# Performance work log

Hardware: AMD Instinct MI355X
Metric: run time of the kernel (lower is better)

The kernel has to match this reference:

```python
import jax, jax.numpy as jnp
import numpy as np

R = 16
ALPHA = 1
SCALING = ALPHA / R
IN_M, IN_N = 64, 64    # factorization(4096)
OUT_L, OUT_K = 64, 64  # factorization(4096)


def setup_inputs() -> dict:
    key = jax.random.key(0)
    k_x, k1a, k1b, k2a, k2b = jax.random.split(key, 5)
    x = jax.random.normal(k_x, (8192, 4096), dtype=jnp.float32)
    # lokr_w1_a: (r, out_l), lokr_w1_b: (in_m, r), lokr_w2_a: (r, out_k), lokr_w2_b: (in_n, r)
    # (init_weights zeros w1_a; we use random values so the test exercises real math)
    s = 0.05
    w1_a = jax.random.normal(k1a, (R, OUT_L), dtype=jnp.float32) * s
    w1_b = jax.random.normal(k1b, (IN_M, R), dtype=jnp.float32) * s
    w2_a = jax.random.normal(k2a, (R, OUT_K), dtype=jnp.float32) * s
    w2_b = jax.random.normal(k2b, (IN_N, R), dtype=jnp.float32) * s
    return {"x": x, "w1_a": w1_a, "w1_b": w1_b, "w2_a": w2_a, "w2_b": w2_b}


def reference(x, w1_a, w1_b, w2_a, w2_b):
    # w1 = w1_a^T @ w1_b^T -> (out_l, in_m); w2 = w2_a^T @ w2_b^T -> (out_k, in_n)
    w1 = w1_a.T @ w1_b.T
    w2 = w2_a.T @ w2_b.T
    # kron(w1^T, w2^T): (in_m*in_n, out_l*out_k) = (in_features, out_features)
    W = jnp.kron(w1.T, w2.T)
    # dropout rate is 0.0 -> identity
    return (x @ W) * SCALING
```

## Files before the change

### kernel.cpp

```cpp
#include <hip/hip_runtime.h>


typedef __fp16 h2 __attribute__((ext_vector_type(2)));
typedef __fp16 h4 __attribute__((ext_vector_type(4)));
typedef float  f4 __attribute__((ext_vector_type(4)));

__device__ __forceinline__ h4 pack4(float a, float b, float c, float d) {
    h2 lo = __builtin_amdgcn_cvt_pkrtz(a, b);
    h2 hi = __builtin_amdgcn_cvt_pkrtz(c, d);
    h4 r;
    r[0] = lo[0]; r[1] = lo[1]; r[2] = hi[0]; r[3] = hi[1];
    return r;
}

#define MFMA16(a, b, c) __builtin_amdgcn_mfma_f32_16x16x16f16((a), (b), (c), 0, 0, 0)

#define ROWS 2

__global__ __launch_bounds__(256) void lokr_kernel(
    const float* __restrict__ x,
    const float* __restrict__ w1_a,
    const float* __restrict__ w1_b,
    const float* __restrict__ w2_a,
    const float* __restrict__ w2_b,
    float* __restrict__ out)
{
    const int lane = threadIdx.x & 63;
    const int g    = lane >> 4;
    const int c    = lane & 15;
    const int gw   = blockIdx.x * 4 + (threadIdx.x >> 6);
    const size_t b0 = (size_t)gw * ROWS;

    h4 W1B[4], W2BT[4], W2A[4], W1AT[4];
#pragma unroll
    for (int t = 0; t < 4; ++t) {
        const int kb = t * 16 + g * 4;
        W1B[t]  = pack4(w1_b[(kb+0)*16 + c], w1_b[(kb+1)*16 + c],
                        w1_b[(kb+2)*16 + c], w1_b[(kb+3)*16 + c]);
        W2BT[t] = pack4(w2_b[(kb+0)*16 + c], w2_b[(kb+1)*16 + c],
                        w2_b[(kb+2)*16 + c], w2_b[(kb+3)*16 + c]);
        W2A[t]  = pack4(w2_a[(g*4+0)*64 + t*16 + c], w2_a[(g*4+1)*64 + t*16 + c],
                        w2_a[(g*4+2)*64 + t*16 + c], w2_a[(g*4+3)*64 + t*16 + c]);
        W1AT[t] = pack4(w1_a[(g*4+0)*64 + t*16 + c] * 0.0625f,
                        w1_a[(g*4+1)*64 + t*16 + c] * 0.0625f,
                        w1_a[(g*4+2)*64 + t*16 + c] * 0.0625f,
                        w1_a[(g*4+3)*64 + t*16 + c] * 0.0625f);
    }

    const f4 zero = {0.f, 0.f, 0.f, 0.f};

#pragma unroll 1
    for (int rr = 0; rr < ROWS; ++rr) {
        const float* xp = x + (b0 + rr) * 4096;

        float xf[4][4][4];
#pragma unroll
        for (int nt = 0; nt < 4; ++nt)
#pragma unroll
            for (int ks = 0; ks < 4; ++ks)
#pragma unroll
                for (int j = 0; j < 4; ++j)
                    xf[nt][ks][j] = xp[(ks*16 + g*4 + j)*64 + nt*16 + c];

        h4 XA[4][4];
#pragma unroll
        for (int nt = 0; nt < 4; ++nt)
#pragma unroll
            for (int ks = 0; ks < 4; ++ks)
                XA[nt][ks] = pack4(xf[nt][ks][0], xf[nt][ks][1],
                                   xf[nt][ks][2], xf[nt][ks][3]);

        f4 PT[4];
#pragma unroll
        for (int nt = 0; nt < 4; ++nt) {
            f4 acc = zero;
#pragma unroll
            for (int ks = 0; ks < 4; ++ks)
                acc = MFMA16(XA[nt][ks], W1B[ks], acc);
            PT[nt] = acc;
        }

        h4 PTH[4];
#pragma unroll
        for (int nt = 0; nt < 4; ++nt)
            PTH[nt] = pack4(PT[nt][0], PT[nt][1], PT[nt][2], PT[nt][3]);
        f4 qa = zero;
#pragma unroll
        for (int nt = 0; nt < 4; ++nt)
            qa = MFMA16(W2BT[nt], PTH[nt], qa);
        h4 QTH = pack4(qa[0], qa[1], qa[2], qa[3]);

        h4 UH[4];
#pragma unroll
        for (int kt = 0; kt < 4; ++kt) {
            f4 u = MFMA16(QTH, W2A[kt], zero);
            UH[kt] = pack4(u[0], u[1], u[2], u[3]);
        }

        float* op = out + (b0 + rr) * 4096 + g * 256 + c;
#pragma unroll
        for (int lt = 0; lt < 4; ++lt) {
#pragma unroll
            for (int kt = 0; kt < 4; ++kt) {
                f4 y = MFMA16(W1AT[lt], UH[kt], zero);
#pragma unroll
                for (int reg = 0; reg < 4; ++reg)
                    op[lt*1024 + reg*64 + kt*16] = y[reg];
            }
        }
    }
}

extern "C" void kernel_launch(void* const* d_in, const int* in_sizes, int n_in,
                              void* d_out, int out_size, void* d_ws, size_t ws_size,
                              hipStream_t stream) {
    const float* x    = (const float*)d_in[0];
    const float* w1_a = (const float*)d_in[1];
    const float* w1_b = (const float*)d_in[2];
    const float* w2_a = (const float*)d_in[3];
    const float* w2_b = (const float*)d_in[4];
    float* out = (float*)d_out;

    dim3 grid(1024), block(256);
    hipLaunchKernelGGL(lokr_kernel, grid, block, 0, stream,
                       x, w1_a, w1_b, w2_a, w2_b, out);
}
```

Baseline: 50.23 us.

## Reorder contraction to use vectorized x loads and prefetch second row

```diff
diff --git a/kernel.cpp b/kernel.cpp
--- a/kernel.cpp
+++ b/kernel.cpp
@@ -15,8 +15,6 @@
 
 #define MFMA16(a, b, c) __builtin_amdgcn_mfma_f32_16x16x16f16((a), (b), (c), 0, 0, 0)
 
-#define ROWS 2
-
 __global__ __launch_bounds__(256) void lokr_kernel(
     const float* __restrict__ x,
     const float* __restrict__ w1_a,
@@ -29,86 +27,88 @@
     const int g    = lane >> 4;
     const int c    = lane & 15;
     const int gw   = blockIdx.x * 4 + (threadIdx.x >> 6);
-    const size_t b0 = (size_t)gw * ROWS;
+    const size_t b0 = (size_t)gw * 2;
 
-    h4 W1B[4], W2BT[4], W2A[4], W1AT[4];
+    h4 W2B[4], W1BT[4], W1A[4], W2A[4];
 #pragma unroll
     for (int t = 0; t < 4; ++t) {
         const int kb = t * 16 + g * 4;
-        W1B[t]  = pack4(w1_b[(kb+0)*16 + c], w1_b[(kb+1)*16 + c],
+        W2B[t]  = pack4(w2_b[(kb+0)*16 + c], w2_b[(kb+1)*16 + c],
+                        w2_b[(kb+2)*16 + c], w2_b[(kb+3)*16 + c]);
+        W1BT[t] = pack4(w1_b[(kb+0)*16 + c], w1_b[(kb+1)*16 + c],
                         w1_b[(kb+2)*16 + c], w1_b[(kb+3)*16 + c]);
-        W2BT[t] = pack4(w2_b[(kb+0)*16 + c], w2_b[(kb+1)*16 + c],
-                        w2_b[(kb+2)*16 + c], w2_b[(kb+3)*16 + c]);
-        W2A[t]  = pack4(w2_a[(g*4+0)*64 + t*16 + c], w2_a[(g*4+1)*64 + t*16 + c],
-                        w2_a[(g*4+2)*64 + t*16 + c], w2_a[(g*4+3)*64 + t*16 + c]);
-        W1AT[t] = pack4(w1_a[(g*4+0)*64 + t*16 + c] * 0.0625f,
+        W1A[t]  = pack4(w1_a[(g*4+0)*64 + t*16 + c] * 0.0625f,
                         w1_a[(g*4+1)*64 + t*16 + c] * 0.0625f,
                         w1_a[(g*4+2)*64 + t*16 + c] * 0.0625f,
                         w1_a[(g*4+3)*64 + t*16 + c] * 0.0625f);
+        W2A[t]  = pack4(w2_a[(g*4+0)*64 + t*16 + c], w2_a[(g*4+1)*64 + t*16 + c],
+                        w2_a[(g*4+2)*64 + t*16 + c], w2_a[(g*4+3)*64 + t*16 + c]);
     }
 
     const f4 zero = {0.f, 0.f, 0.f, 0.f};
 
-#pragma unroll 1
-    for (int rr = 0; rr < ROWS; ++rr) {
-        const float* xp = x + (b0 + rr) * 4096;
+    const float* xp0 = x + b0 * 4096;
+    const float* xp1 = xp0 + 4096;
+    const int xoff = c * 64 + g * 4;
 
-        float xf[4][4][4];
+    auto compute_store = [&](const h4* XA, float* opb) {
+        f4 D1[4];
 #pragma unroll
-        for (int nt = 0; nt < 4; ++nt)
+        for (int mt = 0; mt < 4; ++mt) {
+            f4 a = zero;
 #pragma unroll
-            for (int ks = 0; ks < 4; ++ks)
+            for (int nk = 0; nk < 4; ++nk)
+                a = MFMA16(XA[mt * 4 + nk], W2B[nk], a);
+            D1[mt] = a;
+        }
+        f4 d2 = zero;
 #pragma unroll
-                for (int j = 0; j < 4; ++j)
-                    xf[nt][ks][j] = xp[(ks*16 + g*4 + j)*64 + nt*16 + c];
-
-        h4 XA[4][4];
+        for (int mt = 0; mt < 4; ++mt)
+            d2 = MFMA16(W1BT[mt], pack4(D1[mt][0], D1[mt][1], D1[mt][2], D1[mt][3]), d2);
+        h4 D2H = pack4(d2[0], d2[1], d2[2], d2[3]);
+        h4 D3H[4];
 #pragma unroll
-        for (int nt = 0; nt < 4; ++nt)
-#pragma unroll
-            for (int ks = 0; ks < 4; ++ks)
-                XA[nt][ks] = pack4(xf[nt][ks][0], xf[nt][ks][1],
-                                   xf[nt][ks][2], xf[nt][ks][3]);
-
-        f4 PT[4];
-#pragma unroll
-        for (int nt = 0; nt < 4; ++nt) {
-            f4 acc = zero;
-#pragma unroll
-            for (int ks = 0; ks < 4; ++ks)
-                acc = MFMA16(XA[nt][ks], W1B[ks], acc);
-            PT[nt] = acc;
+        for (int lt = 0; lt < 4; ++lt) {
+            f4 d3 = MFMA16(D2H, W1A[lt], zero);
+            D3H[lt] = pack4(d3[0], d3[1], d3[2], d3[3]);
         }
-
-        h4 PTH[4];
-#pragma unroll
-        for (int nt = 0; nt < 4; ++nt)
-            PTH[nt] = pack4(PT[nt][0], PT[nt][1], PT[nt][2], PT[nt][3]);
-        f4 qa = zero;
-#pragma unroll
-        for (int nt = 0; nt < 4; ++nt)
-            qa = MFMA16(W2BT[nt], PTH[nt], qa);
-        h4 QTH = pack4(qa[0], qa[1], qa[2], qa[3]);
-
-        h4 UH[4];
-#pragma unroll
-        for (int kt = 0; kt < 4; ++kt) {
-            f4 u = MFMA16(QTH, W2A[kt], zero);
-            UH[kt] = pack4(u[0], u[1], u[2], u[3]);
-        }
-
-        float* op = out + (b0 + rr) * 4096 + g * 256 + c;
+        float* op = opb + g * 256 + c;
 #pragma unroll
         for (int lt = 0; lt < 4; ++lt) {
 #pragma unroll
             for (int kt = 0; kt < 4; ++kt) {
-                f4 y = MFMA16(W1AT[lt], UH[kt], zero);
+                f4 y = MFMA16(D3H[lt], W2A[kt], zero);
 #pragma unroll
                 for (int reg = 0; reg < 4; ++reg)
-                    op[lt*1024 + reg*64 + kt*16] = y[reg];
+                    op[lt * 1024 + reg * 64 + kt * 16] = y[reg];
             }
         }
-    }
+    };
+
+    f4 xf[16];
+    h4 XA[16];
+
+#pragma unroll
+    for (int mt = 0; mt < 4; ++mt)
+#pragma unroll
+        for (int nk = 0; nk < 4; ++nk)
+            xf[mt * 4 + nk] = *(const f4*)&xp0[mt * 1024 + nk * 16 + xoff];
+#pragma unroll
+    for (int i = 0; i < 16; ++i)
+        XA[i] = pack4(xf[i][0], xf[i][1], xf[i][2], xf[i][3]);
+#pragma unroll
+    for (int mt = 0; mt < 4; ++mt)
+#pragma unroll
+        for (int nk = 0; nk < 4; ++nk)
+            xf[mt * 4 + nk] = *(const f4*)&xp1[mt * 1024 + nk * 16 + xoff];
+    __builtin_amdgcn_sched_barrier(0);
+
+    compute_store(XA, out + b0 * 4096);
+
+#pragma unroll
+    for (int i = 0; i < 16; ++i)
+        XA[i] = pack4(xf[i][0], xf[i][1], xf[i][2], xf[i][3]);
+    compute_store(XA, out + (b0 + 1) * 4096);
 }
 
 extern "C" void kernel_launch(void* const* d_in, const int* in_sizes, int n_in,
```

Result: faster. 49.00 us (-2.4%).
